# Optimization experiments

Measured on AMD Instinct MI355X. Metric: run time of the kernel, lower is better.

The kernel has to match this reference:

```python
import jax, jax.numpy as jnp
import numpy as np
from jax import lax

B, C, T = 16, 1, 1048576
LEVEL = 5
SELECTED = (3, 4, 5)  # indices into [h1,h2,h3,h4,h5,lowpass5]

SYM4_LO = np.array([-0.07576571478927333, -0.02963552764599851, 0.49761866763201545,
                    0.8037387518059161, 0.29785779560527736, -0.09921954357684722,
                    -0.012603967262037833, 0.032223100604071304], dtype=np.float32)
SYM4_HI = np.array([-0.032223100604071304, -0.012603967262037833, 0.09921954357684722,
                    0.29785779560527736, -0.8037387518059161, 0.49761866763201545,
                    0.02963552764599851, -0.07576571478927333], dtype=np.float32)


def setup_inputs() -> dict:
    key = jax.random.key(0)
    x = jax.random.normal(key, (B, C, T), dtype=jnp.float32)
    return {"x": x, "lowpass": jnp.asarray(SYM4_LO), "highpass": jnp.asarray(SYM4_HI)}


def _circ_conv(x, w):
    # torch: circular pad by L//2 each side, then valid cross-correlation (conv1d).
    pad = w.shape[0] // 2  # 4 for sym4
    xp = jnp.pad(x, ((0, 0), (0, 0), (pad, pad)), mode="wrap")  # (B,1,T+2*pad)
    # lax conv is cross-correlation (no kernel flip), matching torch conv1d.
    return lax.conv_general_dilated(
        xp, w[None, None, :].astype(x.dtype), window_strides=(1,),
        padding="VALID", dimension_numbers=("NCH", "OIH", "NCH"))  # (B,1,T+1)


def reference(x, lowpass, highpass):
    T_in = x.shape[-1]
    coeffs = []
    cur = x
    for _ in range(LEVEL):  # fixed small level loop, not a data-dim loop
        lo = _circ_conv(cur, lowpass)[..., :T_in]
        hi = _circ_conv(cur, highpass)[..., :T_in]
        coeffs.append(hi)
        cur = lo
    coeffs.append(cur[..., :T_in])  # final lowpass approximation
    # include_lowpass=True: pop(-1)+append(-1) is a no-op on ordering.
    out = jnp.stack([coeffs[i] for i in SELECTED], axis=2)  # (B,1,3,T)
    return out
```

## Files before the change

kernel.cpp:

```cpp
#include <hip/hip_runtime.h>


#define TILE      1024
#define NCHUNK    265
#define TPB_TILES 8

typedef float f4v __attribute__((ext_vector_type(4)));

static constexpr float SYM4_LO[8] = {
    -0.07576571478927333f, -0.02963552764599851f, 0.49761866763201545f,
     0.8037387518059161f,   0.29785779560527736f, -0.09921954357684722f,
    -0.012603967262037833f, 0.032223100604071304f};
static constexpr float SYM4_HI[8] = {
    -0.032223100604071304f, -0.012603967262037833f, 0.09921954357684722f,
     0.29785779560527736f,  -0.8037387518059161f,   0.49761866763201545f,
     0.02963552764599851f,  -0.07576571478927333f};

struct FiltPack {
    float f4[36];
    float f5[36];
    float fl[36];
};

constexpr FiltPack make_filters() {
    double lo[8], hi[8];
    for (int i = 0; i < 8; ++i) { lo[i] = SYM4_LO[i]; hi[i] = SYM4_HI[i]; }
    double l2[15] = {}, l3[22] = {}, l4[29] = {};
    for (int i = 0; i < 8;  ++i) for (int j = 0; j < 8; ++j) l2[i + j] += lo[i] * lo[j];
    for (int i = 0; i < 15; ++i) for (int j = 0; j < 8; ++j) l3[i + j] += l2[i] * lo[j];
    for (int i = 0; i < 22; ++i) for (int j = 0; j < 8; ++j) l4[i + j] += l3[i] * lo[j];
    double f4[29] = {}, f5[36] = {}, fl[36] = {};
    for (int i = 0; i < 22; ++i) for (int j = 0; j < 8; ++j) f4[i + j] += l3[i] * hi[j];
    for (int i = 0; i < 29; ++i) for (int j = 0; j < 8; ++j) f5[i + j] += l4[i] * hi[j];
    for (int i = 0; i < 29; ++i) for (int j = 0; j < 8; ++j) fl[i + j] += l4[i] * lo[j];
    FiltPack r = {};
    for (int m = 0; m < 36; ++m) {
        r.f4[m] = (m >= 4 && m < 33) ? (float)f4[m - 4] : 0.0f;
        r.f5[m] = (float)f5[m];
        r.fl[m] = (float)fl[m];
    }
    return r;
}
static constexpr FiltPack FP = make_filters();

__global__ __launch_bounds__(256)
void modwt_fused_kernel(const float* __restrict__ x, float* __restrict__ out,
                        int Tn, int tilesPerRow, int totalTiles) {
    const int T4  = Tn >> 2;
    const int tid = threadIdx.x;
    const bool have2 = (tid < NCHUNK - 256);

    __shared__ f4v s4[NCHUNK];

    const f4v* xbase = reinterpret_cast<const f4v*>(x);
    f4v* o4 = reinterpret_cast<f4v*>(out);

    int tile = blockIdx.x;

    f4v c0, c1;
    {
        const int b   = tile / tilesPerRow;
        const int bs4 = (tile % tilesPerRow) * (TILE / 4);
        const f4v* xr = xbase + (size_t)b * T4;
        int g0 = bs4 - 5 + tid;           if (g0 < 0)   g0 += T4;
        c0 = xr[g0];
        if (have2) { int g1 = bs4 - 5 + 256 + tid; if (g1 >= T4) g1 -= T4; c1 = xr[g1]; }
    }

    for (int k = 0; k < TPB_TILES; ++k) {
        const int b   = tile / tilesPerRow;
        const int bs4 = (tile % tilesPerRow) * (TILE / 4);

        __syncthreads();
        s4[tid] = c0;
        if (have2) s4[256 + tid] = c1;

        const int ntile = tile + gridDim.x;
        if (ntile < totalTiles) {
            const int nb   = ntile / tilesPerRow;
            const int nbs4 = (ntile % tilesPerRow) * (TILE / 4);
            const f4v* xr = xbase + (size_t)nb * T4;
            int g0 = nbs4 - 5 + tid;          if (g0 < 0)   g0 += T4;
            c0 = xr[g0];
            if (have2) { int g1 = nbs4 - 5 + 256 + tid; if (g1 >= T4) g1 -= T4; c1 = xr[g1]; }
        }
        __syncthreads();

        float w[40];
        #pragma unroll
        for (int j = 0; j < 10; ++j)
            reinterpret_cast<f4v*>(w)[j] = s4[tid + j];

        float a4[4] = {0.f, 0.f, 0.f, 0.f};
        float a5[4] = {0.f, 0.f, 0.f, 0.f};
        float al[4] = {0.f, 0.f, 0.f, 0.f};
        #pragma unroll
        for (int m = 0; m < 36; ++m) {
            const float c4v = FP.f4[m];
            const float c5v = FP.f5[m];
            const float clv = FP.fl[m];
            #pragma unroll
            for (int j = 0; j < 4; ++j) {
                const float xv = w[m + j];
                if (c4v != 0.0f) a4[j] = fmaf(c4v, xv, a4[j]);
                a5[j] = fmaf(c5v, xv, a5[j]);
                al[j] = fmaf(clv, xv, al[j]);
            }
        }

        const size_t base = ((size_t)b * 3) * T4 + bs4 + tid;
        f4v v4 = {a4[0], a4[1], a4[2], a4[3]};
        f4v v5 = {a5[0], a5[1], a5[2], a5[3]};
        f4v vl = {al[0], al[1], al[2], al[3]};
        __builtin_nontemporal_store(v4, &o4[base]);
        __builtin_nontemporal_store(v5, &o4[base + T4]);
        __builtin_nontemporal_store(vl, &o4[base + 2 * (size_t)T4]);

        tile = ntile;
    }
}

extern "C" void kernel_launch(void* const* d_in, const int* in_sizes, int n_in,
                              void* d_out, int out_size, void* d_ws, size_t ws_size,
                              hipStream_t stream) {
    const float* x = (const float*)d_in[0];
    float* out = (float*)d_out;
    const int B  = 16;
    const int Tn = in_sizes[0] / B;
    const int tilesPerRow = Tn / TILE;
    const int totalTiles  = B * tilesPerRow;

    dim3 grid(totalTiles / TPB_TILES);
    dim3 block(256);
    modwt_fused_kernel<<<grid, block, 0, stream>>>(x, out, Tn, tilesPerRow, totalTiles);
}
```

Measured before the change: 52.79 us.

## Replace LDS-staged persistent tiles with direct per-thread global window loads

Drops the shared-memory staging, the software-prefetch loop over multiple tiles and the block barriers. Each thread now reads its own 40-sample window straight from global memory, with a wrap-around path only at row edges, and one thread is launched per output quad. This removes the syncthreads and LDS traffic but makes each input element be loaded about ten times through L1/L2 instead of once, and it raises the block count eightfold.

```diff
diff --git a/kernel.cpp b/kernel.cpp
--- a/kernel.cpp
+++ b/kernel.cpp
@@ -1,9 +1,5 @@
 #include <hip/hip_runtime.h>
 
-
-#define TILE      1024
-#define NCHUNK    265
-#define TPB_TILES 8
 
 typedef float f4v __attribute__((ext_vector_type(4)));
 
@@ -44,80 +40,55 @@
 static constexpr FiltPack FP = make_filters();
 
 __global__ __launch_bounds__(256)
-void modwt_fused_kernel(const float* __restrict__ x, float* __restrict__ out,
-                        int Tn, int tilesPerRow, int totalTiles) {
-    const int T4  = Tn >> 2;
-    const int tid = threadIdx.x;
-    const bool have2 = (tid < NCHUNK - 256);
+void modwt_direct_kernel(const float* __restrict__ x, float* __restrict__ out, int Tn) {
+    const int T4 = Tn >> 2;
+    const int g  = blockIdx.x * 256 + threadIdx.x;
+    const int b  = g / T4;
+    const int c  = g - b * T4;
 
-    __shared__ f4v s4[NCHUNK];
+    const f4v* xr = reinterpret_cast<const f4v*>(x) + (size_t)b * T4;
 
-    const f4v* xbase = reinterpret_cast<const f4v*>(x);
-    f4v* o4 = reinterpret_cast<f4v*>(out);
-
-    int tile = blockIdx.x;
-
-    f4v c0, c1;
-    {
-        const int b   = tile / tilesPerRow;
-        const int bs4 = (tile % tilesPerRow) * (TILE / 4);
-        const f4v* xr = xbase + (size_t)b * T4;
-        int g0 = bs4 - 5 + tid;           if (g0 < 0)   g0 += T4;
-        c0 = xr[g0];
-        if (have2) { int g1 = bs4 - 5 + 256 + tid; if (g1 >= T4) g1 -= T4; c1 = xr[g1]; }
+    float w[40];
+    if (c >= 5 && c + 5 <= T4) {
+        const f4v* p = xr + (c - 5);
+        #pragma unroll
+        for (int j = 0; j < 10; ++j)
+            reinterpret_cast<f4v*>(w)[j] = p[j];
+    } else {
+        #pragma unroll
+        for (int j = 0; j < 10; ++j) {
+            int gc = c - 5 + j;
+            if (gc < 0)    gc += T4;
+            if (gc >= T4)  gc -= T4;
+            reinterpret_cast<f4v*>(w)[j] = xr[gc];
+        }
     }
 
-    for (int k = 0; k < TPB_TILES; ++k) {
-        const int b   = tile / tilesPerRow;
-        const int bs4 = (tile % tilesPerRow) * (TILE / 4);
+    float a4[4] = {0.f, 0.f, 0.f, 0.f};
+    float a5[4] = {0.f, 0.f, 0.f, 0.f};
+    float al[4] = {0.f, 0.f, 0.f, 0.f};
+    #pragma unroll
+    for (int m = 0; m < 36; ++m) {
+        const float c4v = FP.f4[m];
+        const float c5v = FP.f5[m];
+        const float clv = FP.fl[m];
+        #pragma unroll
+        for (int j = 0; j < 4; ++j) {
+            const float xv = w[m + j];
+            if (c4v != 0.0f) a4[j] = fmaf(c4v, xv, a4[j]);
+            a5[j] = fmaf(c5v, xv, a5[j]);
+            al[j] = fmaf(clv, xv, al[j]);
+        }
+    }
 
-        __syncthreads();
-        s4[tid] = c0;
-        if (have2) s4[256 + tid] = c1;
-
-        const int ntile = tile + gridDim.x;
-        if (ntile < totalTiles) {
-            const int nb   = ntile / tilesPerRow;
-            const int nbs4 = (ntile % tilesPerRow) * (TILE / 4);
-            const f4v* xr = xbase + (size_t)nb * T4;
-            int g0 = nbs4 - 5 + tid;          if (g0 < 0)   g0 += T4;
-            c0 = xr[g0];
-            if (have2) { int g1 = nbs4 - 5 + 256 + tid; if (g1 >= T4) g1 -= T4; c1 = xr[g1]; }
-        }
-        __syncthreads();
-
-        float w[40];
-        #pragma unroll
-        for (int j = 0; j < 10; ++j)
-            reinterpret_cast<f4v*>(w)[j] = s4[tid + j];
-
-        float a4[4] = {0.f, 0.f, 0.f, 0.f};
-        float a5[4] = {0.f, 0.f, 0.f, 0.f};
-        float al[4] = {0.f, 0.f, 0.f, 0.f};
-        #pragma unroll
-        for (int m = 0; m < 36; ++m) {
-            const float c4v = FP.f4[m];
-            const float c5v = FP.f5[m];
-            const float clv = FP.fl[m];
-            #pragma unroll
-            for (int j = 0; j < 4; ++j) {
-                const float xv = w[m + j];
-                if (c4v != 0.0f) a4[j] = fmaf(c4v, xv, a4[j]);
-                a5[j] = fmaf(c5v, xv, a5[j]);
-                al[j] = fmaf(clv, xv, al[j]);
-            }
-        }
-
-        const size_t base = ((size_t)b * 3) * T4 + bs4 + tid;
-        f4v v4 = {a4[0], a4[1], a4[2], a4[3]};
-        f4v v5 = {a5[0], a5[1], a5[2], a5[3]};
-        f4v vl = {al[0], al[1], al[2], al[3]};
-        __builtin_nontemporal_store(v4, &o4[base]);
-        __builtin_nontemporal_store(v5, &o4[base + T4]);
-        __builtin_nontemporal_store(vl, &o4[base + 2 * (size_t)T4]);
-
-        tile = ntile;
-    }
+    f4v* o4 = reinterpret_cast<f4v*>(out);
+    const size_t base = ((size_t)b * 3) * T4 + c;
+    f4v v4 = {a4[0], a4[1], a4[2], a4[3]};
+    f4v v5 = {a5[0], a5[1], a5[2], a5[3]};
+    f4v vl = {al[0], al[1], al[2], al[3]};
+    __builtin_nontemporal_store(v4, &o4[base]);
+    __builtin_nontemporal_store(v5, &o4[base + T4]);
+    __builtin_nontemporal_store(vl, &o4[base + 2 * (size_t)T4]);
 }
 
 extern "C" void kernel_launch(void* const* d_in, const int* in_sizes, int n_in,
@@ -127,10 +98,9 @@
     float* out = (float*)d_out;
     const int B  = 16;
     const int Tn = in_sizes[0] / B;
-    const int tilesPerRow = Tn / TILE;
-    const int totalTiles  = B * tilesPerRow;
+    const int totalQuads = B * (Tn / 4);
 
-    dim3 grid(totalTiles / TPB_TILES);
+    dim3 grid(totalQuads / 256);
     dim3 block(256);
-    modwt_fused_kernel<<<grid, block, 0, stream>>>(x, out, Tn, tilesPerRow, totalTiles);
+    modwt_direct_kernel<<<grid, block, 0, stream>>>(x, out, Tn);
 }
```

Result: faster. 51.17 us (-3.1%).
